# Performance work log

Hardware: AMD Instinct MI355X
Metric: run time of the kernel (lower is better)

The kernel has to match this reference:

```python
import jax, jax.numpy as jnp
import numpy as np

N = 1048576
FEA = 128
N0 = 16384


def setup_inputs() -> dict:
    key = jax.random.key(0)
    k1, k2 = jax.random.split(key)
    atom_fea = jax.random.normal(k1, (N, FEA), dtype=jnp.float32)
    segment_ids = jnp.sort(jax.random.randint(k2, (N,), 0, N0, dtype=jnp.int32))
    return {"atom_fea": atom_fea, "segment_ids": segment_ids, "num_crystals": N0}


def reference(atom_fea, segment_ids, num_crystals):
    # Fused segment-mean: equivalent to [mean(atom_fea[idx]) for idx in crystal_atom_idx]
    sums = jax.ops.segment_sum(atom_fea, segment_ids, num_segments=num_crystals)  # (N0, FEA)
    counts = jax.ops.segment_sum(jnp.ones((atom_fea.shape[0],), atom_fea.dtype),
                                 segment_ids, num_segments=num_crystals)  # (N0,)
    counts = jnp.maximum(counts, 1.0)  # guard empty segments (original assumes none)
    return sums / counts[:, None]
```

## Files before the change

kernel.cpp:

```cpp
#include <hip/hip_runtime.h>

#define FEA   128
#define CHUNK 256

typedef float f4 __attribute__((ext_vector_type(4)));

__global__ __launch_bounds__(256) void prologue_kernel(
    const int* __restrict__ ids, int* __restrict__ B, float* __restrict__ out,
    int n_atoms, int n_seg, int b_blocks, int n_chunks)
{
    if ((int)blockIdx.x < b_blocks) {
        const int t  = blockIdx.x * 256 + threadIdx.x;
        const int i0 = t * 4;
        if (i0 >= n_atoms) return;
        int prev = (i0 == 0) ? -1 : ids[i0 - 1];
        #pragma unroll
        for (int j = 0; j < 4; ++j) {
            const int i = i0 + j;
            if (i >= n_atoms) break;
            const int cur = ids[i];
            if (cur != prev) {
                for (int s = prev + 1; s <= cur; ++s) B[s] = i;
                for (int s = prev + 1; s < cur; ++s) {
                    f4* row = (f4*)(out + (size_t)s * FEA);
                    const f4 z = {0.f, 0.f, 0.f, 0.f};
                    for (int q = 0; q < FEA / 4; ++q) row[q] = z;
                }
                prev = cur;
            }
        }
        if (i0 + 4 >= n_atoms) {
            for (int s = prev + 1; s <= n_seg; ++s) B[s] = n_atoms;
            for (int s = prev + 1; s < n_seg; ++s) {
                f4* row = (f4*)(out + (size_t)s * FEA);
                const f4 z = {0.f, 0.f, 0.f, 0.f};
                for (int q = 0; q < FEA / 4; ++q) row[q] = z;
            }
        }
    } else {
        const int t = ((int)blockIdx.x - b_blocks) * 256 + threadIdx.x;
        const int b = t >> 5;
        const int g = t & 31;
        const int p = (b + 1) * CHUNK;
        if (b >= n_chunks - 1 || p >= n_atoms) return;
        if (ids[p - 1] == ids[p]) {
            const f4 z = {0.f, 0.f, 0.f, 0.f};
            ((f4*)(out + (size_t)ids[p] * FEA))[g] = z;
        }
    }
}

__global__ void segmean_chunk_kernel(
    const float* __restrict__ atom_fea,
    const int*   __restrict__ ids,
    const int*   __restrict__ B,
    float*       __restrict__ out,
    int n_atoms)
{
    const int wid   = (blockIdx.x * 256 + threadIdx.x) >> 6;
    const int lane  = threadIdx.x & 63;
    const int c0    = wid * CHUNK;
    if (c0 >= n_atoms) return;
    const int c1    = min(c0 + CHUNK, n_atoms);
    const int a_sub = lane >> 5;
    const int g     = lane & 31;

    int s   = ids[c0];
    int pos = c0;

    while (pos < c1) {
        const int segS = B[s];
        const int segE = B[s + 1];
        const int e    = min(segE, c1);
        const int m    = e - pos;

        const f4* base = (const f4*)atom_fea + (size_t)pos * (FEA / 4) + g;

        f4 a0 = {0.f, 0.f, 0.f, 0.f};
        f4 a1 = {0.f, 0.f, 0.f, 0.f};
        f4 a2 = {0.f, 0.f, 0.f, 0.f};
        f4 a3 = {0.f, 0.f, 0.f, 0.f};

        int k = a_sub;
        for (; k + 14 < m; k += 16) {
            f4 v0 = base[(size_t)(k     ) * 32];
            f4 v1 = base[(size_t)(k +  2) * 32];
            f4 v2 = base[(size_t)(k +  4) * 32];
            f4 v3 = base[(size_t)(k +  6) * 32];
            f4 v4 = base[(size_t)(k +  8) * 32];
            f4 v5 = base[(size_t)(k + 10) * 32];
            f4 v6 = base[(size_t)(k + 12) * 32];
            f4 v7 = base[(size_t)(k + 14) * 32];
            a0 += v0; a1 += v1; a2 += v2; a3 += v3;
            a0 += v4; a1 += v5; a2 += v6; a3 += v7;
        }
        for (; k + 6 < m; k += 8) {
            f4 v0 = base[(size_t)(k    ) * 32];
            f4 v1 = base[(size_t)(k + 2) * 32];
            f4 v2 = base[(size_t)(k + 4) * 32];
            f4 v3 = base[(size_t)(k + 6) * 32];
            a0 += v0; a1 += v1; a2 += v2; a3 += v3;
        }
        for (; k < m; k += 2)
            a0 += base[(size_t)k * 32];

        a0 += a1 + a2 + a3;

        a0[0] += __shfl_xor(a0[0], 32, 64);
        a0[1] += __shfl_xor(a0[1], 32, 64);
        a0[2] += __shfl_xor(a0[2], 32, 64);
        a0[3] += __shfl_xor(a0[3], 32, 64);

        const int   n_total = segE - segS;
        const float invn    = 1.0f / (float)((n_total > 0) ? n_total : 1);

        if (segS >= c0 && segE <= c1) {
            if (a_sub == 0) {
                f4 r = a0 * invn;
                ((f4*)(out + (size_t)s * FEA))[g] = r;
            }
        } else {
            if (a_sub == 0) {
                float* dst = out + (size_t)s * FEA + g * 4;
                atomicAdd(dst + 0, a0[0] * invn);
                atomicAdd(dst + 1, a0[1] * invn);
                atomicAdd(dst + 2, a0[2] * invn);
                atomicAdd(dst + 3, a0[3] * invn);
            }
        }
        pos = e;
        ++s;
    }
}

__global__ __launch_bounds__(256) void segmean_bsearch_kernel(
    const float* __restrict__ atom_fea,
    const int*   __restrict__ ids,
    float*       __restrict__ out,
    int n_atoms, int n_seg)
{
    const int wave = threadIdx.x >> 6;
    const int lane = threadIdx.x & 63;
    const int seg  = blockIdx.x * 4 + wave;
    if (seg >= n_seg) return;

    int lo0 = 0, hi0 = n_atoms, lo1 = 0, hi1 = n_atoms;
    while ((lo0 < hi0) | (lo1 < hi1)) {
        if (lo0 < hi0) { int m = (lo0 + hi0) >> 1; if (ids[m] < seg)     lo0 = m + 1; else hi0 = m; }
        if (lo1 < hi1) { int m = (lo1 + hi1) >> 1; if (ids[m] < seg + 1) lo1 = m + 1; else hi1 = m; }
    }
    const int start = lo0;
    const int n     = lo1 - lo0;

    const int a_sub = lane >> 5;
    const int g     = lane & 31;
    const f4* base  = (const f4*)atom_fea + (size_t)start * (FEA / 4) + g;

    f4 a0 = {0.f, 0.f, 0.f, 0.f};
    for (int k = a_sub; k < n; k += 2)
        a0 += base[(size_t)k * 32];

    a0[0] += __shfl_xor(a0[0], 32, 64);
    a0[1] += __shfl_xor(a0[1], 32, 64);
    a0[2] += __shfl_xor(a0[2], 32, 64);
    a0[3] += __shfl_xor(a0[3], 32, 64);

    const float invn = 1.0f / (float)((n > 0) ? n : 1);
    if (a_sub == 0) {
        f4 r = a0 * invn;
        ((f4*)(out + (size_t)seg * FEA))[g] = r;
    }
}

extern "C" void kernel_launch(void* const* d_in, const int* in_sizes, int n_in,
                              void* d_out, int out_size, void* d_ws, size_t ws_size,
                              hipStream_t stream) {
    const float* atom_fea = (const float*)d_in[0];
    const int*   ids      = (const int*)d_in[1];
    float*       out      = (float*)d_out;

    const int n_atoms = in_sizes[1];
    const int n_seg   = out_size / FEA;

    const size_t bounds_bytes = (size_t)(n_seg + 1) * sizeof(int);
    const int    n_chunks     = (n_atoms + CHUNK - 1) / CHUNK;

    if (ws_size >= bounds_bytes) {
        int* B = (int*)d_ws;

        const int b_blocks = (((n_atoms + 3) / 4) + 255) / 256;
        const int z_thr    = (n_chunks > 1) ? (n_chunks - 1) * 32 : 0;
        const int z_blocks = (z_thr + 255) / 256;

        prologue_kernel<<<b_blocks + z_blocks, 256, 0, stream>>>(
            ids, B, out, n_atoms, n_seg, b_blocks, n_chunks);

        const int m_blocks = (n_chunks + 3) / 4;
        segmean_chunk_kernel<<<m_blocks, 256, 0, stream>>>(
            atom_fea, ids, B, out, n_atoms);
    } else {
        const int seg_blocks = (n_seg + 3) / 4;
        segmean_bsearch_kernel<<<seg_blocks, 256, 0, stream>>>(
            atom_fea, ids, out, n_atoms, n_seg);
    }
}
```

Measured before the change: 118.5 us.

## Assign each segment to the chunk containing its start, drop atomics and zeroing

```diff
diff --git a/kernel.cpp b/kernel.cpp
--- a/kernel.cpp
+++ b/kernel.cpp
@@ -1,80 +1,73 @@
 #include <hip/hip_runtime.h>
 
 #define FEA   128
-#define CHUNK 256
+#define CHUNK 128
 
 typedef float f4 __attribute__((ext_vector_type(4)));
 
-__global__ __launch_bounds__(256) void prologue_kernel(
-    const int* __restrict__ ids, int* __restrict__ B, float* __restrict__ out,
-    int n_atoms, int n_seg, int b_blocks, int n_chunks)
+__global__ __launch_bounds__(256) void bounds_kernel(
+    const int* __restrict__ ids, int* __restrict__ B, int n_atoms, int n_seg)
 {
-    if ((int)blockIdx.x < b_blocks) {
-        const int t  = blockIdx.x * 256 + threadIdx.x;
-        const int i0 = t * 4;
-        if (i0 >= n_atoms) return;
-        int prev = (i0 == 0) ? -1 : ids[i0 - 1];
+    const int t  = blockIdx.x * 256 + threadIdx.x;
+    const int i0 = t * 4;
+    if (i0 >= n_atoms) return;
+
+    int prev = (i0 == 0) ? -1 : ids[i0 - 1];
+
+    if (i0 + 3 < n_atoms) {
+        const int4 v = *(const int4*)(ids + i0);
+        const int cur[4] = {v.x, v.y, v.z, v.w};
         #pragma unroll
         for (int j = 0; j < 4; ++j) {
-            const int i = i0 + j;
-            if (i >= n_atoms) break;
-            const int cur = ids[i];
-            if (cur != prev) {
-                for (int s = prev + 1; s <= cur; ++s) B[s] = i;
-                for (int s = prev + 1; s < cur; ++s) {
-                    f4* row = (f4*)(out + (size_t)s * FEA);
-                    const f4 z = {0.f, 0.f, 0.f, 0.f};
-                    for (int q = 0; q < FEA / 4; ++q) row[q] = z;
-                }
-                prev = cur;
+            if (cur[j] != prev) {
+                for (int s = prev + 1; s <= cur[j]; ++s) B[s] = i0 + j;
+                prev = cur[j];
             }
         }
-        if (i0 + 4 >= n_atoms) {
+        if (i0 + 4 == n_atoms)
             for (int s = prev + 1; s <= n_seg; ++s) B[s] = n_atoms;
-            for (int s = prev + 1; s < n_seg; ++s) {
-                f4* row = (f4*)(out + (size_t)s * FEA);
-                const f4 z = {0.f, 0.f, 0.f, 0.f};
-                for (int q = 0; q < FEA / 4; ++q) row[q] = z;
+    } else {
+        for (int j = 0; j < 4 && i0 + j < n_atoms; ++j) {
+            const int c = ids[i0 + j];
+            if (c != prev) {
+                for (int s = prev + 1; s <= c; ++s) B[s] = i0 + j;
+                prev = c;
             }
         }
-    } else {
-        const int t = ((int)blockIdx.x - b_blocks) * 256 + threadIdx.x;
-        const int b = t >> 5;
-        const int g = t & 31;
-        const int p = (b + 1) * CHUNK;
-        if (b >= n_chunks - 1 || p >= n_atoms) return;
-        if (ids[p - 1] == ids[p]) {
-            const f4 z = {0.f, 0.f, 0.f, 0.f};
-            ((f4*)(out + (size_t)ids[p] * FEA))[g] = z;
-        }
+        for (int s = prev + 1; s <= n_seg; ++s) B[s] = n_atoms;
     }
 }
 
-__global__ void segmean_chunk_kernel(
+__global__ void segmean_aligned_kernel(
     const float* __restrict__ atom_fea,
-    const int*   __restrict__ ids,
     const int*   __restrict__ B,
     float*       __restrict__ out,
-    int n_atoms)
+    int n_atoms, int n_seg, int n_chunks)
 {
-    const int wid   = (blockIdx.x * 256 + threadIdx.x) >> 6;
-    const int lane  = threadIdx.x & 63;
-    const int c0    = wid * CHUNK;
-    if (c0 >= n_atoms) return;
-    const int c1    = min(c0 + CHUNK, n_atoms);
+    const int wid  = (blockIdx.x * 256 + threadIdx.x) >> 6;
+    if (wid >= n_chunks) return;
+    const int lane = threadIdx.x & 63;
+
+    const int  c0   = wid * CHUNK;
+    const int  c1   = min(c0 + CHUNK, n_atoms);
+    const bool last = (wid == n_chunks - 1);
+
+    int lo = 0, hi = n_seg + 1;
+    while (lo < hi) {
+        const int mid = (lo + hi) >> 1;
+        if (B[mid] < c0) lo = mid + 1; else hi = mid;
+    }
+
     const int a_sub = lane >> 5;
     const int g     = lane & 31;
 
-    int s   = ids[c0];
-    int pos = c0;
+    for (int s = lo; s < n_seg; ++s) {
+        const int segS = B[s];
+        if (last ? (segS > c1) : (segS >= c1)) break;
+        const int segE = B[s + 1];
+        const int n    = segE - segS;
 
-    while (pos < c1) {
-        const int segS = B[s];
-        const int segE = B[s + 1];
-        const int e    = min(segE, c1);
-        const int m    = e - pos;
-
-        const f4* base = (const f4*)atom_fea + (size_t)pos * (FEA / 4) + g;
+        const f4* base = (const f4*)atom_fea + (size_t)segS * (FEA / 4) + g;
 
         f4 a0 = {0.f, 0.f, 0.f, 0.f};
         f4 a1 = {0.f, 0.f, 0.f, 0.f};
@@ -82,26 +75,14 @@
         f4 a3 = {0.f, 0.f, 0.f, 0.f};
 
         int k = a_sub;
-        for (; k + 14 < m; k += 16) {
-            f4 v0 = base[(size_t)(k     ) * 32];
-            f4 v1 = base[(size_t)(k +  2) * 32];
-            f4 v2 = base[(size_t)(k +  4) * 32];
-            f4 v3 = base[(size_t)(k +  6) * 32];
-            f4 v4 = base[(size_t)(k +  8) * 32];
-            f4 v5 = base[(size_t)(k + 10) * 32];
-            f4 v6 = base[(size_t)(k + 12) * 32];
-            f4 v7 = base[(size_t)(k + 14) * 32];
-            a0 += v0; a1 += v1; a2 += v2; a3 += v3;
-            a0 += v4; a1 += v5; a2 += v6; a3 += v7;
-        }
-        for (; k + 6 < m; k += 8) {
+        for (; k + 6 < n; k += 8) {
             f4 v0 = base[(size_t)(k    ) * 32];
             f4 v1 = base[(size_t)(k + 2) * 32];
             f4 v2 = base[(size_t)(k + 4) * 32];
             f4 v3 = base[(size_t)(k + 6) * 32];
             a0 += v0; a1 += v1; a2 += v2; a3 += v3;
         }
-        for (; k < m; k += 2)
+        for (; k < n; k += 2)
             a0 += base[(size_t)k * 32];
 
         a0 += a1 + a2 + a3;
@@ -111,25 +92,12 @@
         a0[2] += __shfl_xor(a0[2], 32, 64);
         a0[3] += __shfl_xor(a0[3], 32, 64);
 
-        const int   n_total = segE - segS;
-        const float invn    = 1.0f / (float)((n_total > 0) ? n_total : 1);
+        const float invn = 1.0f / (float)((n > 0) ? n : 1);
 
-        if (segS >= c0 && segE <= c1) {
-            if (a_sub == 0) {
-                f4 r = a0 * invn;
-                ((f4*)(out + (size_t)s * FEA))[g] = r;
-            }
-        } else {
-            if (a_sub == 0) {
-                float* dst = out + (size_t)s * FEA + g * 4;
-                atomicAdd(dst + 0, a0[0] * invn);
-                atomicAdd(dst + 1, a0[1] * invn);
-                atomicAdd(dst + 2, a0[2] * invn);
-                atomicAdd(dst + 3, a0[3] * invn);
-            }
+        if (a_sub == 0) {
+            f4 r = a0 * invn;
+            ((f4*)(out + (size_t)s * FEA))[g] = r;
         }
-        pos = e;
-        ++s;
     }
 }
 
@@ -189,15 +157,11 @@
         int* B = (int*)d_ws;
 
         const int b_blocks = (((n_atoms + 3) / 4) + 255) / 256;
-        const int z_thr    = (n_chunks > 1) ? (n_chunks - 1) * 32 : 0;
-        const int z_blocks = (z_thr + 255) / 256;
-
-        prologue_kernel<<<b_blocks + z_blocks, 256, 0, stream>>>(
-            ids, B, out, n_atoms, n_seg, b_blocks, n_chunks);
+        bounds_kernel<<<b_blocks, 256, 0, stream>>>(ids, B, n_atoms, n_seg);
 
         const int m_blocks = (n_chunks + 3) / 4;
-        segmean_chunk_kernel<<<m_blocks, 256, 0, stream>>>(
-            atom_fea, ids, B, out, n_atoms);
+        segmean_aligned_kernel<<<m_blocks, 256, 0, stream>>>(
+            atom_fea, B, out, n_atoms, n_seg, n_chunks);
     } else {
         const int seg_blocks = (n_seg + 3) / 4;
         segmean_bsearch_kernel<<<seg_blocks, 256, 0, stream>>>(
```

New measurement: 117.9 us. No clear change (-0.5%).
